# Kernel optimization log

Measured on AMD Instinct MI355X. Metric: run time of the kernel, lower is better.

The kernel has to match this reference:

```python
import jax, jax.numpy as jnp
import numpy as np

UNITS = 512
EPS = 1e-6

def setup_inputs() -> dict:
    key = jax.random.key(0)
    x = jax.random.normal(key, (262144, UNITS), dtype=jnp.float32)
    return {"x": x}

def reference(x):
    d = x.shape[1]
    # Gram matrix with diagonal jitter: [d, d]
    g = x.T @ x + jnp.eye(d, dtype=x.dtype) * EPS
    L = jnp.linalg.cholesky(g)  # lower triangular [d, d]
    # inv(L) via triangular solve (same math as tf.linalg.inv on L)
    L_inv = jax.scipy.linalg.solve_triangular(L, jnp.eye(d, dtype=x.dtype), lower=True)
    ortho_weights = L_inv.T * jnp.sqrt(jnp.float32(UNITS))
    return x @ ortho_weights
```

## Files before the change

kernel.cpp:

```cpp
#include <hip/hip_runtime.h>


#define EPSJ 1e-6f
#define SQRTD 22.627416997969522f

typedef short bf16x8 __attribute__((ext_vector_type(8)));
typedef float f32x4 __attribute__((ext_vector_type(4)));

__device__ __forceinline__ unsigned short f2bf(float f) {
  unsigned u = __float_as_uint(f);
  unsigned r = u + 0x7fffu + ((u >> 16) & 1u);
  return (unsigned short)(r >> 16);
}

__device__ __forceinline__ int swz(int row, int slot) {
  return slot ^ ((row ^ (row >> 3)) & 7);
}

#define GLOAD16(g, l)                                                         \
  __builtin_amdgcn_global_load_lds(                                           \
      (const __attribute__((address_space(1))) void*)(g),                     \
      (__attribute__((address_space(3))) void*)(l), 16, 0, 0)

__global__ __launch_bounds__(512, 2) void gram_k1(
    const float* __restrict__ X, unsigned short* __restrict__ Xbf,
    float* __restrict__ part, int nchunk) {
  __shared__ unsigned short As[256 * 64];
  __shared__ unsigned short Bs[256 * 64];
  const int b = blockIdx.x;
  const int s0 = (int)((long)4096 * b / nchunk);
  const int s1 = (int)((long)4096 * (b + 1) / nchunk);
  const int t = threadIdx.x, lane = t & 63, w = t >> 6;
  const int wr = w >> 2, wc = w & 3;
  const int kg = t >> 6;
  const int c = t & 63;
  unsigned short* half = (c < 32) ? As : Bs;
  const int cl = (c & 31) * 8;

  f32x4 acc[8][4];
  const f32x4 zf = {0.f, 0.f, 0.f, 0.f};
  #pragma unroll
  for (int a = 0; a < 8; ++a)
    #pragma unroll
    for (int bb = 0; bb < 4; ++bb) acc[a][bb] = zf;

  for (int ks = s0; ks < s1; ++ks) {
    long r0 = (long)ks * 64 + kg * 8;
    const float* src = X + r0 * 512 + c * 8;
    uint4 rp[8];
    #pragma unroll
    for (int rr = 0; rr < 8; ++rr) {
      float4 f0 = *(const float4*)(src + rr * 512);
      float4 f1 = *(const float4*)(src + rr * 512 + 4);
      rp[rr].x = (unsigned)f2bf(f0.x) | ((unsigned)f2bf(f0.y) << 16);
      rp[rr].y = (unsigned)f2bf(f0.z) | ((unsigned)f2bf(f0.w) << 16);
      rp[rr].z = (unsigned)f2bf(f1.x) | ((unsigned)f2bf(f1.y) << 16);
      rp[rr].w = (unsigned)f2bf(f1.z) | ((unsigned)f2bf(f1.w) << 16);
      *(uint4*)(Xbf + (r0 + rr) * 512 + c * 8) = rp[rr];
    }
    #pragma unroll
    for (int s = 0; s < 8; ++s) {
      unsigned v[8];
      #pragma unroll
      for (int rr = 0; rr < 8; ++rr) {
        unsigned word = (s & 4) ? ((s & 2) ? rp[rr].w : rp[rr].z)
                                : ((s & 2) ? rp[rr].y : rp[rr].x);
        v[rr] = (s & 1) ? (word >> 16) : (word & 0xFFFFu);
      }
      uint4 o = make_uint4(v[0] | (v[1] << 16), v[2] | (v[3] << 16),
                           v[4] | (v[5] << 16), v[6] | (v[7] << 16));
      int cc = cl + s;
      int sl = kg ^ ((cc ^ (cc >> 3)) & 7);
      *(uint4*)((char*)half + cc * 128 + sl * 16) = o;
    }
    __syncthreads();
    #pragma unroll
    for (int kk = 0; kk < 2; ++kk) {
      bf16x8 af[8], bfr[4];
      #pragma unroll
      for (int fm = 0; fm < 8; ++fm) {
        int row = wr * 128 + fm * 16 + (lane & 15);
        af[fm] = *(const bf16x8*)((const char*)As + row * 128 +
                                  swz(row, kk * 4 + (lane >> 4)) * 16);
      }
      #pragma unroll
      for (int fn = 0; fn < 4; ++fn) {
        int row = wc * 64 + fn * 16 + (lane & 15);
        bfr[fn] = *(const bf16x8*)((const char*)Bs + row * 128 +
                                   swz(row, kk * 4 + (lane >> 4)) * 16);
      }
      #pragma unroll
      for (int fm = 0; fm < 8; ++fm)
        #pragma unroll
        for (int fn = 0; fn < 4; ++fn)
          acc[fm][fn] = __builtin_amdgcn_mfma_f32_16x16x32_bf16(
              bfr[fn], af[fm], acc[fm][fn], 0, 0, 0);
    }
    __syncthreads();
  }
  float* out = part + (long)(b * 3 + 2) * 65536;
  #pragma unroll
  for (int fm = 0; fm < 8; ++fm)
    #pragma unroll
    for (int fn = 0; fn < 4; ++fn) {
      int mi = wr * 128 + fm * 16 + (lane & 15);
      int nj = wc * 64 + fn * 16 + (lane >> 4) * 4;
      *(float4*)(out + mi * 256 + nj) = *(float4*)&acc[fm][fn];
    }
}

__device__ __forceinline__ void stage_pack4(
    const unsigned short* __restrict__ src, unsigned short* dst, int c0,
    int kg) {
  uint4 r0 = *(const uint4*)src;
  uint4 r1 = *(const uint4*)(src + 512);
  uint4 r2 = *(const uint4*)(src + 1024);
  uint4 r3 = *(const uint4*)(src + 1536);
  unsigned a[4] = {r0.x, r0.y, r0.z, r0.w};
  unsigned b[4] = {r1.x, r1.y, r1.z, r1.w};
  unsigned c[4] = {r2.x, r2.y, r2.z, r2.w};
  unsigned d[4] = {r3.x, r3.y, r3.z, r3.w};
  const int khi = kg >> 1, koff = (kg & 1) * 8;
  #pragma unroll
  for (int s = 0; s < 8; ++s) {
    int wsel = s >> 1, sh = (s & 1) * 16;
    unsigned v0 = (a[wsel] >> sh) & 0xFFFFu;
    unsigned v1 = (b[wsel] >> sh) & 0xFFFFu;
    unsigned v2 = (c[wsel] >> sh) & 0xFFFFu;
    unsigned v3 = (d[wsel] >> sh) & 0xFFFFu;
    int cc = c0 + s;
    int sl = khi ^ ((cc ^ (cc >> 3)) & 7);
    *(uint2*)((char*)dst + cc * 128 + sl * 16 + koff) =
        make_uint2(v0 | (v1 << 16), v2 | (v3 << 16));
  }
}

__global__ __launch_bounds__(512, 2) void gram_k2(
    const unsigned short* __restrict__ Xbf, float* __restrict__ part,
    int nchunk) {
  __shared__ unsigned short As[256 * 64];
  const int b = blockIdx.x, pos = b & 1, chunk = b >> 1;
  const int s0 = (int)((long)4096 * chunk / nchunk);
  const int s1 = (int)((long)4096 * (chunk + 1) / nchunk);
  const int ca = pos ? 256 : 0;
  const int t = threadIdx.x, lane = t & 63, w = t >> 6;
  const int wr = w >> 2, wc = w & 3;

  f32x4 acc[8][4];
  const f32x4 zf = {0.f, 0.f, 0.f, 0.f};
  #pragma unroll
  for (int a = 0; a < 8; ++a)
    #pragma unroll
    for (int bb = 0; bb < 4; ++bb) acc[a][bb] = zf;

  const int c0 = (t & 31) * 8;
  const int kg = t >> 5;

  for (int ks = s0; ks < s1; ++ks) {
    long r = (long)ks * 64 + kg * 4;
    stage_pack4(Xbf + r * 512 + ca + c0, As, c0, kg);
    __syncthreads();
    #pragma unroll
    for (int kk = 0; kk < 2; ++kk) {
      bf16x8 af[8], bfr[4];
      #pragma unroll
      for (int fm = 0; fm < 8; ++fm) {
        int row = wr * 128 + fm * 16 + (lane & 15);
        af[fm] = *(const bf16x8*)((const char*)As + row * 128 +
                                  swz(row, kk * 4 + (lane >> 4)) * 16);
      }
      #pragma unroll
      for (int fn = 0; fn < 4; ++fn) {
        int row = wc * 64 + fn * 16 + (lane & 15);
        bfr[fn] = *(const bf16x8*)((const char*)As + row * 128 +
                                   swz(row, kk * 4 + (lane >> 4)) * 16);
      }
      #pragma unroll
      for (int fm = 0; fm < 8; ++fm)
        #pragma unroll
        for (int fn = 0; fn < 4; ++fn)
          acc[fm][fn] = __builtin_amdgcn_mfma_f32_16x16x32_bf16(
              bfr[fn], af[fm], acc[fm][fn], 0, 0, 0);
    }
    __syncthreads();
  }
  float* out = part + (long)(chunk * 3 + pos) * 65536;
  #pragma unroll
  for (int fm = 0; fm < 8; ++fm)
    #pragma unroll
    for (int fn = 0; fn < 4; ++fn) {
      int mi = wr * 128 + fm * 16 + (lane & 15);
      int nj = wc * 64 + fn * 16 + (lane >> 4) * 4;
      *(float4*)(out + mi * 256 + nj) = *(float4*)&acc[fm][fn];
    }
}

__global__ __launch_bounds__(512, 2) void gram_f32(
    const float* __restrict__ X, float* __restrict__ part, int nchunk) {
  __shared__ unsigned short As[256 * 64];
  __shared__ unsigned short Bs[256 * 64];
  const int b = blockIdx.x;
  const int pos = b % 3;
  const int chunk = b / 3;
  const int CR = 262144 / nchunk;
  const long r0 = (long)chunk * CR;
  const int ca = (pos == 1) ? 256 : 0;
  const int cb = (pos == 0) ? 0 : 256;
  const bool diag = (pos != 2);
  const int t = threadIdx.x, lane = t & 63, w = t >> 6;
  const int wr = w >> 2, wc = w & 3;

  f32x4 acc[8][4];
  const f32x4 zf = {0.f, 0.f, 0.f, 0.f};
  #pragma unroll
  for (int a = 0; a < 8; ++a)
    #pragma unroll
    for (int bb = 0; bb < 4; ++bb) acc[a][bb] = zf;

  const int c_oct = t & 31, msub = t >> 5;

  for (int ks = 0; ks < CR; ks += 64) {
    #pragma unroll
    for (int it = 0; it < 4; ++it) {
      int m = msub + 16 * it;
      long row = r0 + ks + m;
      const float4* sa = (const float4*)(X + row * 512 + ca + c_oct * 8);
      float4 a0 = sa[0], a1 = sa[1];
      {
        float v[8] = {a0.x, a0.y, a0.z, a0.w, a1.x, a1.y, a1.z, a1.w};
        #pragma unroll
        for (int s = 0; s < 8; ++s) {
          int cc = c_oct * 8 + s;
          int off = cc * 128 + ((2 * m) ^ (((cc ^ (cc >> 3)) & 7) << 4));
          *(unsigned short*)((char*)As + off) = f2bf(v[s]);
        }
      }
      if (!diag) {
        const float4* sb = (const float4*)(X + row * 512 + cb + c_oct * 8);
        float4 b0 = sb[0], b1 = sb[1];
        float v[8] = {b0.x, b0.y, b0.z, b0.w, b1.x, b1.y, b1.z, b1.w};
        #pragma unroll
        for (int s = 0; s < 8; ++s) {
          int cc = c_oct * 8 + s;
          int off = cc * 128 + ((2 * m) ^ (((cc ^ (cc >> 3)) & 7) << 4));
          *(unsigned short*)((char*)Bs + off) = f2bf(v[s]);
        }
      }
    }
    __syncthreads();
    const unsigned short* Bp = diag ? As : Bs;
    #pragma unroll
    for (int kk = 0; kk < 2; ++kk) {
      bf16x8 af[8], bfr[4];
      #pragma unroll
      for (int fm = 0; fm < 8; ++fm) {
        int row = wr * 128 + fm * 16 + (lane & 15);
        af[fm] = *(const bf16x8*)((const char*)As + row * 128 +
                                  swz(row, kk * 4 + (lane >> 4)) * 16);
      }
      #pragma unroll
      for (int fn = 0; fn < 4; ++fn) {
        int row = wc * 64 + fn * 16 + (lane & 15);
        bfr[fn] = *(const bf16x8*)((const char*)Bp + row * 128 +
                                   swz(row, kk * 4 + (lane >> 4)) * 16);
      }
      #pragma unroll
      for (int fm = 0; fm < 8; ++fm)
        #pragma unroll
        for (int fn = 0; fn < 4; ++fn)
          acc[fm][fn] = __builtin_amdgcn_mfma_f32_16x16x32_bf16(
              bfr[fn], af[fm], acc[fm][fn], 0, 0, 0);
    }
    __syncthreads();
  }
  float* out = part + (long)b * 65536;
  #pragma unroll
  for (int fm = 0; fm < 8; ++fm)
    #pragma unroll
    for (int fn = 0; fn < 4; ++fn) {
      int mi = wr * 128 + fm * 16 + (lane & 15);
      int nj = wc * 64 + fn * 16 + (lane >> 4) * 4;
      *(float4*)(out + mi * 256 + nj) = *(float4*)&acc[fm][fn];
    }
}

__global__ void gram_reduce(const float* __restrict__ part,
                            float* __restrict__ G, int nchunk) {
  int idx = blockIdx.x * 256 + threadIdx.x;
  int pos = idx >> 16;
  int e = idx & 65535;
  float s = 0.f;
  for (int ch = 0; ch < nchunk; ++ch)
    s += part[(long)(ch * 3 + pos) * 65536 + e];
  int i = e >> 8, j = e & 255;
  if (pos == 0) {
    G[i * 512 + j] = s;
  } else if (pos == 1) {
    G[(256 + i) * 512 + 256 + j] = s;
  } else {
    G[i * 512 + 256 + j] = s;
    G[(256 + j) * 512 + i] = s;
  }
}

__global__ __launch_bounds__(256) void chol_step(float* __restrict__ G,
                                                 float* __restrict__ Dinv,
                                                 int p) {
  __shared__ float Pb[64][65];
  __shared__ float Sb[64][65];
  __shared__ float Inv[64][65];
  __shared__ float SbP[64][65];
  __shared__ float Ub[64][65];
  __shared__ float Tt[32][33];
  const int t = threadIdx.x;
  const int r0 = 64 * p;
  const int tr = (t >> 4) * 4, tc = (t & 15) * 4;

  for (int idx = t; idx < 4096; idx += 256) {
    int i = idx >> 6, j = idx & 63;
    float v = G[(long)(r0 + i) * 512 + r0 + j];
    if (i == j) v += EPSJ;
    Pb[i][j] = v;
  }
  __syncthreads();

  if (p > 0) {
    float cc[4][4] = {{0.f}};
    for (int r = 0; r < p; ++r) {
      for (int idx = t; idx < 4096; idx += 256) {
        int i = idx >> 6, j = idx & 63;
        Sb[i][j] = G[(long)(r0 + i) * 512 + 64 * r + j];
      }
      __syncthreads();
      #pragma unroll 4
      for (int k = 0; k < 64; ++k) {
        float a0 = Sb[tr][k], a1 = Sb[tr+1][k], a2 = Sb[tr+2][k], a3 = Sb[tr+3][k];
        float b0 = Sb[tc][k], b1 = Sb[tc+1][k], b2 = Sb[tc+2][k], b3 = Sb[tc+3][k];
        cc[0][0]+=a0*b0; cc[0][1]+=a0*b1; cc[0][2]+=a0*b2; cc[0][3]+=a0*b3;
        cc[1][0]+=a1*b0; cc[1][1]+=a1*b1; cc[1][2]+=a1*b2; cc[1][3]+=a1*b3;
        cc[2][0]+=a2*b0; cc[2][1]+=a2*b1; cc[2][2]+=a2*b2; cc[2][3]+=a2*b3;
        cc[3][0]+=a3*b0; cc[3][1]+=a3*b1; cc[3][2]+=a3*b2; cc[3][3]+=a3*b3;
      }
      __syncthreads();
    }
    #pragma unroll
    for (int u = 0; u < 4; ++u)
      #pragma unroll
      for (int v = 0; v < 4; ++v)
        Pb[tr + u][tc + v] -= cc[u][v];
    __syncthreads();
  }

  const int lane = t & 63, w = t >> 6;
  #pragma unroll
  for (int sp = 0; sp < 2; ++sp) {
    const int b0 = sp * 32;
    if (w == 0) {
      float rr[32];
      #pragma unroll
      for (int k = 0; k < 32; ++k)
        rr[k] = (lane < 32) ? Pb[b0 + lane][b0 + k] : 0.f;
      #pragma unroll
      for (int j = 0; j < 32; ++j) {
        float d = sqrtf(__shfl(rr[j], j));
        if (lane == j) rr[j] = d;
        else if (lane > j && lane < 32) rr[j] = rr[j] / d;
        float rj = rr[j];
        #pragma unroll
        for (int k = j + 1; k < 32; ++k) {
          float Lkj = __shfl(rj, k);
          if (lane > j && lane < 32) rr[k] -= rj * Lkj;
        }
      }
      #pragma unroll
      for (int k = 0; k < 32; ++k)
        if (lane < 32) Pb[b0 + lane][b0 + k] = rr[k];
    }
    __syncthreads();
    if (sp == 0) {
      if (t < 32) {
        int rw = 32 + t;
        float x[32];
        #pragma unroll
        for (int j = 0; j < 32; ++j) x[j] = Pb[rw][j];
        #pragma unroll
        for (int j = 0; j < 32; ++j) {
          float xj = x[j] / Pb[j][j];
          x[j] = xj;
          #pragma unroll
          for (int k2 = j + 1; k2 < 32; ++k2) x[k2] -= xj * Pb[k2][j];
        }
        #pragma unroll
        for (int j = 0; j < 32; ++j) Pb[rw][j] = x[j];
      }
      __syncthreads();
      {
        int i = 32 + (t >> 3), kb = 32 + (t & 7) * 4;
        float sv[4];
        #pragma unroll
        for (int e = 0; e < 4; ++e) sv[e] = Pb[i][kb + e];
        #pragma unroll 4
        for (int j = 0; j < 32; ++j) {
          float aij = Pb[i][j];
          #pragma unroll
          for (int e = 0; e < 4; ++e) sv[e] -= aij * Pb[kb + e][j];
        }
        #pragma unroll
        for (int e = 0; e < 4; ++e) Pb[i][kb + e] = sv[e];
      }
      __syncthreads();
    }
  }

  if (t < 64) {
    int col = t & 31, o = (t >> 5) * 32;
    float x[32];
    #pragma unroll
    for (int i = 0; i < 32; ++i) {
      float s = (i == col) ? 1.f : 0.f;
      #pragma unroll
      for (int j = 0; j < i; ++j) s -= Pb[o + i][o + j] * x[j];
      x[i] = s / Pb[o + i][o + i];
    }
    #pragma unroll
    for (int i = 0; i < 32; ++i) Inv[o + i][o + col] = x[i];
  }
  for (int idx = t; idx < 1024; idx += 256)
    Inv[idx >> 5][32 + (idx & 31)] = 0.f;
  __syncthreads();
  {
    int i = t >> 3, jb = (t & 7) * 4;
    float sv[4] = {0.f, 0.f, 0.f, 0.f};
    #pragma unroll 4
    for (int k = 0; k < 32; ++k) {
      float bik = Pb[32 + i][k];
      #pragma unroll
      for (int e = 0; e < 4; ++e) sv[e] += bik * Inv[k][jb + e];
    }
    #pragma unroll
    for (int e = 0; e < 4; ++e) Tt[i][jb + e] = sv[e];
  }
  __syncthreads();
  {
    int i = t >> 3, jb = (t & 7) * 4;
    float sv[4] = {0.f, 0.f, 0.f, 0.f};
    #pragma unroll 4
    for (int k = 0; k < 32; ++k) {
      float cik = Inv[32 + i][32 + k];
      #pragma unroll
      for (int e = 0; e < 4; ++e) sv[e] += cik * Tt[k][jb + e];
    }
    #pragma unroll
    for (int e = 0; e < 4; ++e) Inv[32 + i][jb + e] = -sv[e];
  }
  __syncthreads();

  if (blockIdx.x == 0) {
    for (int idx = t; idx < 4096; idx += 256)
      Dinv[p * 4096 + idx] = Inv[idx >> 6][idx & 63];
    return;
  }

  const long rI = 64 * (p + blockIdx.x), cP = 64 * p;
  float cc2[4][4] = {{0.f}};
  for (int r = 0; r < p; ++r) {
    __syncthreads();
    for (int idx = t; idx < 4096; idx += 256) {
      int i = idx >> 6, j = idx & 63;
      Sb[i][j] = G[(rI + i) * 512 + 64 * r + j];
      SbP[i][j] = G[(cP + i) * 512 + 64 * r + j];
    }
    __syncthreads();
    #pragma unroll 4
    for (int k = 0; k < 64; ++k) {
      float a0 = Sb[tr][k], a1 = Sb[tr+1][k], a2 = Sb[tr+2][k], a3 = Sb[tr+3][k];
      float b0 = SbP[tc][k], b1 = SbP[tc+1][k], b2 = SbP[tc+2][k], b3 = SbP[tc+3][k];
      cc2[0][0]+=a0*b0; cc2[0][1]+=a0*b1; cc2[0][2]+=a0*b2; cc2[0][3]+=a0*b3;
      cc2[1][0]+=a1*b0; cc2[1][1]+=a1*b1; cc2[1][2]+=a1*b2; cc2[1][3]+=a1*b3;
      cc2[2][0]+=a2*b0; cc2[2][1]+=a2*b1; cc2[2][2]+=a2*b2; cc2[2][3]+=a2*b3;
      cc2[3][0]+=a3*b0; cc2[3][1]+=a3*b1; cc2[3][2]+=a3*b2; cc2[3][3]+=a3*b3;
    }
  }
  __syncthreads();
  #pragma unroll
  for (int u = 0; u < 4; ++u)
    #pragma unroll
    for (int v = 0; v < 4; ++v)
      Ub[tr + u][tc + v] = G[(rI + tr + u) * 512 + cP + tc + v] - cc2[u][v];
  __syncthreads();
  float xx[4][4] = {{0.f}};
  #pragma unroll 4
  for (int k = 0; k < 64; ++k) {
    float a0 = Ub[tr][k], a1 = Ub[tr+1][k], a2 = Ub[tr+2][k], a3 = Ub[tr+3][k];
    float b0 = Inv[tc][k], b1 = Inv[tc+1][k], b2 = Inv[tc+2][k], b3 = Inv[tc+3][k];
    xx[0][0]+=a0*b0; xx[0][1]+=a0*b1; xx[0][2]+=a0*b2; xx[0][3]+=a0*b3;
    xx[1][0]+=a1*b0; xx[1][1]+=a1*b1; xx[1][2]+=a1*b2; xx[1][3]+=a1*b3;
    xx[2][0]+=a2*b0; xx[2][1]+=a2*b1; xx[2][2]+=a2*b2; xx[2][3]+=a2*b3;
    xx[3][0]+=a3*b0; xx[3][1]+=a3*b1; xx[3][2]+=a3*b2; xx[3][3]+=a3*b3;
  }
  #pragma unroll
  for (int u = 0; u < 4; ++u)
    #pragma unroll
    for (int v = 0; v < 4; ++v)
      G[(rI + tr + u) * 512 + cP + tc + v] = xx[u][v];
}

__global__ __launch_bounds__(256) void tri_assemble(
    const float* __restrict__ G, const float* __restrict__ Dinv,
    unsigned short* __restrict__ Wt) {
  __shared__ float Bsh[448 * 64];
  __shared__ float T[64 * 64];
  const int q = blockIdx.x, t = threadIdx.x;
  const int or_ = (t >> 4) * 4, oc = (t & 15) * 4;

  for (int p = q + 1; p < 8; ++p) {
    float cc[4][4] = {{0.f}};
    for (int r = q; r < p; ++r) {
      const float* Lbase = G + (long)(64 * p) * 512 + 64 * r;
      #pragma unroll 4
      for (int k = 0; k < 64; ++k) {
        float a0 = Lbase[(or_ + 0) * 512 + k];
        float a1 = Lbase[(or_ + 1) * 512 + k];
        float a2 = Lbase[(or_ + 2) * 512 + k];
        float a3 = Lbase[(or_ + 3) * 512 + k];
        float b0, b1, b2, b3;
        if (r == q) {
          const float* Bq = Dinv + q * 4096 + k * 64 + oc;
          b0 = Bq[0]; b1 = Bq[1]; b2 = Bq[2]; b3 = Bq[3];
        } else {
          const float* Br = Bsh + ((r - q - 1) * 64 + k) * 64 + oc;
          b0 = Br[0]; b1 = Br[1]; b2 = Br[2]; b3 = Br[3];
        }
        cc[0][0] += a0*b0; cc[0][1] += a0*b1; cc[0][2] += a0*b2; cc[0][3] += a0*b3;
        cc[1][0] += a1*b0; cc[1][1] += a1*b1; cc[1][2] += a1*b2; cc[1][3] += a1*b3;
        cc[2][0] += a2*b0; cc[2][1] += a2*b1; cc[2][2] += a2*b2; cc[2][3] += a2*b3;
        cc[3][0] += a3*b0; cc[3][1] += a3*b1; cc[3][2] += a3*b2; cc[3][3] += a3*b3;
      }
    }
    #pragma unroll
    for (int u = 0; u < 4; ++u)
      #pragma unroll
      for (int v = 0; v < 4; ++v)
        T[(or_ + u) * 64 + oc + v] = cc[u][v];
    __syncthreads();

    float c2[4][4] = {{0.f}};
    const float* Dp = Dinv + p * 4096;
    #pragma unroll 4
    for (int k = 0; k < 64; ++k) {
      float a0 = Dp[(or_ + 0) * 64 + k];
      float a1 = Dp[(or_ + 1) * 64 + k];
      float a2 = Dp[(or_ + 2) * 64 + k];
      float a3 = Dp[(or_ + 3) * 64 + k];
      const float* Tk = T + k * 64 + oc;
      float b0 = Tk[0], b1 = Tk[1], b2 = Tk[2], b3 = Tk[3];
      c2[0][0] += a0*b0; c2[0][1] += a0*b1; c2[0][2] += a0*b2; c2[0][3] += a0*b3;
      c2[1][0] += a1*b0; c2[1][1] += a1*b1; c2[1][2] += a1*b2; c2[1][3] += a1*b3;
      c2[2][0] += a2*b0; c2[2][1] += a2*b1; c2[2][2] += a2*b2; c2[2][3] += a2*b3;
      c2[3][0] += a3*b0; c2[3][1] += a3*b1; c2[3][2] += a3*b2; c2[3][3] += a3*b3;
    }
    #pragma unroll
    for (int u = 0; u < 4; ++u)
      #pragma unroll
      for (int v = 0; v < 4; ++v)
        Bsh[((p - q - 1) * 64 + or_ + u) * 64 + oc + v] = -c2[u][v];
    __syncthreads();
  }

  const int nr = (8 - q) * 64;
  for (int idx = t; idx < nr * 64; idx += 256) {
    int i = idx >> 6, kk = idx & 63;
    float v = (i < 64) ? Dinv[q * 4096 + i * 64 + kk]
                       : Bsh[(i - 64) * 64 + kk];
    int n = 64 * q + i;
    Wt[(long)n * 512 + 64 * q + kk] = f2bf(SQRTD * v);
  }
  for (int idx = t; idx < 64 * q * 64; idx += 256) {
    int n = idx >> 6, kk = idx & 63;
    Wt[(long)n * 512 + 64 * q + kk] = 0;
  }
}

__global__ __launch_bounds__(512, 4) void ymm5(
    const unsigned short* __restrict__ Xbf,
    const unsigned short* __restrict__ Wt, float* __restrict__ Y) {
  __shared__ unsigned short As[2][128 * 64];
  __shared__ unsigned short Bs[2][128 * 64];
  const int t = threadIdx.x, lane = t & 63, w = t >> 6;
  const int id = blockIdx.x;
  const int xcd = id & 7, j = id >> 3;
  const long m0 = (long)((j >> 2) * 8 + xcd) * 128;
  const int n0 = (j & 3) * 128;
  const int wm = (w >> 1) * 32, wn = (w & 1) * 64;
  f32x4 acc[2][4];
  const f32x4 zf = {0.f, 0.f, 0.f, 0.f};
  #pragma unroll
  for (int a = 0; a < 2; ++a)
    #pragma unroll
    for (int bq = 0; bq < 4; ++bq) acc[a][bq] = zf;

  auto stage = [&](int buf, int k0) {
    #pragma unroll
    for (int h = 0; h < 2; ++h) {
      int seg = t + h * 512;
      int row = seg >> 3, sl = seg & 7;
      const unsigned short* sA =
          Xbf + (m0 + row) * 512 + k0 + swz(row, sl) * 8;
      const unsigned short* sB =
          Wt + (long)(n0 + row) * 512 + k0 + swz(row, sl) * 8;
      GLOAD16(sA, &As[buf][seg * 8]);
      GLOAD16(sB, &Bs[buf][seg * 8]);
    }
  };
  auto compute = [&](int buf) {
    #pragma unroll
    for (int kk = 0; kk < 2; ++kk) {
      bf16x8 af[2], bfr[4];
      #pragma unroll
      for (int fm = 0; fm < 2; ++fm) {
        int row = wm + fm * 16 + (lane & 15);
        af[fm] = *(const bf16x8*)((const char*)As[buf] + row * 128 +
                                  swz(row, kk * 4 + (lane >> 4)) * 16);
      }
      #pragma unroll
      for (int fn = 0; fn < 4; ++fn) {
        int row = wn + fn * 16 + (lane & 15);
        bfr[fn] = *(const bf16x8*)((const char*)Bs[buf] + row * 128 +
                                   swz(row, kk * 4 + (lane >> 4)) * 16);
      }
      #pragma unroll
      for (int fm = 0; fm < 2; ++fm)
        #pragma unroll
        for (int fn = 0; fn < 4; ++fn)
          acc[fm][fn] = __builtin_amdgcn_mfma_f32_16x16x32_bf16(
              bfr[fn], af[fm], acc[fm][fn], 0, 0, 0);
    }
  };

  stage(0, 0);
  asm volatile("s_waitcnt vmcnt(0)" ::: "memory");
  __builtin_amdgcn_s_barrier();
  int cur = 0;
  #pragma unroll 1
  for (int kt = 0; kt < 7; ++kt) {
    stage(cur ^ 1, (kt + 1) * 64);
    asm volatile("s_waitcnt vmcnt(4)" ::: "memory");
    __builtin_amdgcn_sched_barrier(0);
    __builtin_amdgcn_s_barrier();
    compute(cur);
    __builtin_amdgcn_s_barrier();
    cur ^= 1;
  }
  asm volatile("s_waitcnt vmcnt(0)" ::: "memory");
  __builtin_amdgcn_sched_barrier(0);
  __builtin_amdgcn_s_barrier();
  compute(cur);

  #pragma unroll
  for (int fm = 0; fm < 2; ++fm)
    #pragma unroll
    for (int fn = 0; fn < 4; ++fn) {
      long row = m0 + wm + fm * 16 + (lane & 15);
      int col = n0 + wn + fn * 16 + (lane >> 4) * 4;
      *(float4*)(Y + row * 512 + col) = *(float4*)&acc[fm][fn];
    }
}

__global__ __launch_bounds__(256) void ymm_v1(const float* __restrict__ X,
                                              const unsigned short* __restrict__ Wt,
                                              float* __restrict__ Y) {
  __shared__ unsigned short As[128 * 64];
  __shared__ unsigned short Bs[128 * 64];
  const int t = threadIdx.x, lane = t & 63, w = t >> 6;
  const long m0 = (long)blockIdx.x * 128;
  const int n0 = blockIdx.y * 128;
  const int wm = (w >> 1) * 64, wn = (w & 1) * 64;
  f32x4 acc[4][4];
  const f32x4 zf = {0.f, 0.f, 0.f, 0.f};
  #pragma unroll
  for (int a = 0; a < 4; ++a)
    #pragma unroll
    for (int bq = 0; bq < 4; ++bq) acc[a][bq] = zf;
  const int ko = t & 7, mrow = t >> 3;

  for (int k0 = 0; k0 < 512; k0 += 64) {
    #pragma unroll
    for (int it = 0; it < 4; ++it) {
      int m = mrow + 32 * it;
      const float4* src = (const float4*)(X + (m0 + m) * 512 + k0 + ko * 8);
      float4 f0 = src[0], f1 = src[1];
      unsigned p0 = (unsigned)f2bf(f0.x) | ((unsigned)f2bf(f0.y) << 16);
      unsigned p1 = (unsigned)f2bf(f0.z) | ((unsigned)f2bf(f0.w) << 16);
      unsigned p2 = (unsigned)f2bf(f1.x) | ((unsigned)f2bf(f1.y) << 16);
      unsigned p3 = (unsigned)f2bf(f1.z) | ((unsigned)f2bf(f1.w) << 16);
      int slot = swz(m, ko);
      *(uint4*)((char*)As + m * 128 + slot * 16) = make_uint4(p0, p1, p2, p3);
    }
    #pragma unroll
    for (int it = 0; it < 4; ++it) {
      int n = mrow + 32 * it;
      uint4 raw = *(const uint4*)(Wt + (long)(n0 + n) * 512 + k0 + ko * 8);
      int slot = swz(n, ko);
      *(uint4*)((char*)Bs + n * 128 + slot * 16) = raw;
    }
    __syncthreads();
    #pragma unroll
    for (int kk = 0; kk < 2; ++kk) {
      bf16x8 af[4], bfr[4];
      #pragma unroll
      for (int fm = 0; fm < 4; ++fm) {
        int row = wm + fm * 16 + (lane & 15);
        af[fm] = *(const bf16x8*)((const char*)As + row * 128 +
                                  swz(row, kk * 4 + (lane >> 4)) * 16);
      }
      #pragma unroll
      for (int fn = 0; fn < 4; ++fn) {
        int row = wn + fn * 16 + (lane & 15);
        bfr[fn] = *(const bf16x8*)((const char*)Bs + row * 128 +
                                   swz(row, kk * 4 + (lane >> 4)) * 16);
      }
      #pragma unroll
      for (int fm = 0; fm < 4; ++fm)
        #pragma unroll
        for (int fn = 0; fn < 4; ++fn)
          acc[fm][fn] = __builtin_amdgcn_mfma_f32_16x16x32_bf16(
              af[fm], bfr[fn], acc[fm][fn], 0, 0, 0);
    }
    __syncthreads();
  }
  #pragma unroll
  for (int fm = 0; fm < 4; ++fm)
    #pragma unroll
    for (int fn = 0; fn < 4; ++fn)
      #pragma unroll
      for (int j = 0; j < 4; ++j) {
        long row = m0 + wm + fm * 16 + (lane >> 4) * 4 + j;
        int col = n0 + wn + fn * 16 + (lane & 15);
        Y[row * 512 + col] = acc[fm][fn][j];
      }
}

extern "C" void kernel_launch(void* const* d_in, const int* in_sizes, int n_in,
                              void* d_out, int out_size, void* d_ws, size_t ws_size,
                              hipStream_t stream) {
  const float* X = (const float*)d_in[0];
  float* Y = (float*)d_out;
  char* ws = (char*)d_ws;
  float* G = (float*)ws;
  unsigned short* Wt = (unsigned short*)(ws + (1 << 20));
  float* Dinv = (float*)(ws + (1 << 20) + (1 << 19));

  const int NCH = 255;
  size_t part_off = (size_t)(2 << 20);
  size_t part_bytes = (size_t)NCH * 3 * 65536 * 4;
  size_t xbf_off = part_off + part_bytes;
  size_t need = xbf_off + (size_t)134217728 * 2;

  if (ws_size >= need) {
    float* part = (float*)(ws + part_off);
    unsigned short* Xbf = (unsigned short*)(ws + xbf_off);
    gram_k1<<<NCH, 512, 0, stream>>>(X, Xbf, part, NCH);
    gram_k2<<<2 * NCH, 512, 0, stream>>>(Xbf, part, NCH);
    gram_reduce<<<768, 256, 0, stream>>>(part, G, NCH);
    for (int p = 0; p < 8; ++p)
      chol_step<<<8 - p, 256, 0, stream>>>(G, Dinv, p);
    tri_assemble<<<8, 256, 0, stream>>>(G, Dinv, Wt);
    ymm5<<<8192, 512, 0, stream>>>(Xbf, Wt, Y);
  } else {
    float* part = (float*)(ws + part_off);
    size_t fixed = part_off;
    int nchunk = 64;
    while (nchunk > 1 && fixed + (size_t)nchunk * 3 * 65536 * 4 > ws_size)
      nchunk >>= 1;
    gram_f32<<<3 * nchunk, 512, 0, stream>>>(X, part, nchunk);
    gram_reduce<<<768, 256, 0, stream>>>(part, G, nchunk);
    for (int p = 0; p < 8; ++p)
      chol_step<<<8 - p, 256, 0, stream>>>(G, Dinv, p);
    tri_assemble<<<8, 256, 0, stream>>>(G, Dinv, Wt);
    ymm_v1<<<dim3(2048, 4), 256, 0, stream>>>(X, Wt, Y);
  }
}
```

Before: 1.581 ms.

## Split blocked Cholesky step into diagonal and panel kernels, tweak ymm barriers

Each Cholesky step is split into two launches. A single-block kernel factors and inverts the 64x64 diagonal block, then writes the factored block and its inverse to global memory. A second kernel then updates the trailing panel blocks using the stored inverse. Before, every block of the step redundantly recomputed the diagonal factorization. In exchange the number of launches roughly doubles. The ymm kernel also drops its sched_barriers and adds an lgkmcnt wait before the second barrier.

```diff
diff --git a/kernel.cpp b/kernel.cpp
--- a/kernel.cpp
+++ b/kernel.cpp
@@ -15,6 +15,12 @@
 
 __device__ __forceinline__ int swz(int row, int slot) {
   return slot ^ ((row ^ (row >> 3)) & 7);
+}
+
+__device__ __forceinline__ float wred(float s) {
+  s += __shfl_xor(s, 1);  s += __shfl_xor(s, 2);  s += __shfl_xor(s, 4);
+  s += __shfl_xor(s, 8);  s += __shfl_xor(s, 16); s += __shfl_xor(s, 32);
+  return s;
 }
 
 #define GLOAD16(g, l)                                                         \
@@ -255,14 +261,14 @@
       #pragma unroll
       for (int fm = 0; fm < 8; ++fm) {
         int row = wr * 128 + fm * 16 + (lane & 15);
-        af[fm] = *(const bf16x8*)((const char*)As + row * 128 +
-                                  swz(row, kk * 4 + (lane >> 4)) * 16);
+        int slot = swz(row, kk * 4 + (lane >> 4));
+        af[fm] = *(const bf16x8*)((const char*)As + row * 128 + slot * 16);
       }
       #pragma unroll
       for (int fn = 0; fn < 4; ++fn) {
         int row = wc * 64 + fn * 16 + (lane & 15);
-        bfr[fn] = *(const bf16x8*)((const char*)Bp + row * 128 +
-                                   swz(row, kk * 4 + (lane >> 4)) * 16);
+        int slot = swz(row, kk * 4 + (lane >> 4));
+        bfr[fn] = *(const bf16x8*)((const char*)Bp + row * 128 + slot * 16);
       }
       #pragma unroll
       for (int fm = 0; fm < 8; ++fm)
@@ -303,14 +309,12 @@
   }
 }
 
-__global__ __launch_bounds__(256) void chol_step(float* __restrict__ G,
-                                                 float* __restrict__ Dinv,
-                                                 int p) {
+__global__ __launch_bounds__(256) void chol_d64(float* __restrict__ G,
+                                                float* __restrict__ Dinv,
+                                                int p) {
   __shared__ float Pb[64][65];
   __shared__ float Sb[64][65];
   __shared__ float Inv[64][65];
-  __shared__ float SbP[64][65];
-  __shared__ float Ub[64][65];
   __shared__ float Tt[32][33];
   const int t = threadIdx.x;
   const int r0 = 64 * p;
@@ -454,31 +458,44 @@
     for (int e = 0; e < 4; ++e) Inv[32 + i][jb + e] = -sv[e];
   }
   __syncthreads();
-
-  if (blockIdx.x == 0) {
-    for (int idx = t; idx < 4096; idx += 256)
-      Dinv[p * 4096 + idx] = Inv[idx >> 6][idx & 63];
-    return;
-  }
-
-  const long rI = 64 * (p + blockIdx.x), cP = 64 * p;
-  float cc2[4][4] = {{0.f}};
+  for (int idx = t; idx < 4096; idx += 256) {
+    int i = idx >> 6, j = idx & 63;
+    G[(long)(r0 + i) * 512 + r0 + j] = Pb[i][j];
+    Dinv[p * 4096 + idx] = Inv[i][j];
+  }
+}
+
+__global__ __launch_bounds__(256) void chol_t64(float* __restrict__ G,
+                                                const float* __restrict__ Dinv,
+                                                int p) {
+  __shared__ float SbI[64][65];
+  __shared__ float SbP[64][65];
+  __shared__ float Ub[64][65];
+  __shared__ float Db[64][65];
+  const int t = threadIdx.x;
+  const long rI = 64 * (p + 1 + blockIdx.x), cP = 64 * p;
+  const int tr = (t >> 4) * 4, tc = (t & 15) * 4;
+
+  for (int idx = t; idx < 4096; idx += 256)
+    Db[idx >> 6][idx & 63] = Dinv[p * 4096 + idx];
+
+  float cc[4][4] = {{0.f}};
   for (int r = 0; r < p; ++r) {
     __syncthreads();
     for (int idx = t; idx < 4096; idx += 256) {
       int i = idx >> 6, j = idx & 63;
-      Sb[i][j] = G[(rI + i) * 512 + 64 * r + j];
+      SbI[i][j] = G[(rI + i) * 512 + 64 * r + j];
       SbP[i][j] = G[(cP + i) * 512 + 64 * r + j];
     }
     __syncthreads();
     #pragma unroll 4
     for (int k = 0; k < 64; ++k) {
-      float a0 = Sb[tr][k], a1 = Sb[tr+1][k], a2 = Sb[tr+2][k], a3 = Sb[tr+3][k];
+      float a0 = SbI[tr][k], a1 = SbI[tr+1][k], a2 = SbI[tr+2][k], a3 = SbI[tr+3][k];
       float b0 = SbP[tc][k], b1 = SbP[tc+1][k], b2 = SbP[tc+2][k], b3 = SbP[tc+3][k];
-      cc2[0][0]+=a0*b0; cc2[0][1]+=a0*b1; cc2[0][2]+=a0*b2; cc2[0][3]+=a0*b3;
-      cc2[1][0]+=a1*b0; cc2[1][1]+=a1*b1; cc2[1][2]+=a1*b2; cc2[1][3]+=a1*b3;
-      cc2[2][0]+=a2*b0; cc2[2][1]+=a2*b1; cc2[2][2]+=a2*b2; cc2[2][3]+=a2*b3;
-      cc2[3][0]+=a3*b0; cc2[3][1]+=a3*b1; cc2[3][2]+=a3*b2; cc2[3][3]+=a3*b3;
+      cc[0][0]+=a0*b0; cc[0][1]+=a0*b1; cc[0][2]+=a0*b2; cc[0][3]+=a0*b3;
+      cc[1][0]+=a1*b0; cc[1][1]+=a1*b1; cc[1][2]+=a1*b2; cc[1][3]+=a1*b3;
+      cc[2][0]+=a2*b0; cc[2][1]+=a2*b1; cc[2][2]+=a2*b2; cc[2][3]+=a2*b3;
+      cc[3][0]+=a3*b0; cc[3][1]+=a3*b1; cc[3][2]+=a3*b2; cc[3][3]+=a3*b3;
     }
   }
   __syncthreads();
@@ -486,13 +503,14 @@
   for (int u = 0; u < 4; ++u)
     #pragma unroll
     for (int v = 0; v < 4; ++v)
-      Ub[tr + u][tc + v] = G[(rI + tr + u) * 512 + cP + tc + v] - cc2[u][v];
+      Ub[tr + u][tc + v] =
+          G[(rI + tr + u) * 512 + cP + tc + v] - cc[u][v];
   __syncthreads();
   float xx[4][4] = {{0.f}};
   #pragma unroll 4
   for (int k = 0; k < 64; ++k) {
     float a0 = Ub[tr][k], a1 = Ub[tr+1][k], a2 = Ub[tr+2][k], a3 = Ub[tr+3][k];
-    float b0 = Inv[tc][k], b1 = Inv[tc+1][k], b2 = Inv[tc+2][k], b3 = Inv[tc+3][k];
+    float b0 = Db[tc][k], b1 = Db[tc+1][k], b2 = Db[tc+2][k], b3 = Db[tc+3][k];
     xx[0][0]+=a0*b0; xx[0][1]+=a0*b1; xx[0][2]+=a0*b2; xx[0][3]+=a0*b3;
     xx[1][0]+=a1*b0; xx[1][1]+=a1*b1; xx[1][2]+=a1*b2; xx[1][3]+=a1*b3;
     xx[2][0]+=a2*b0; xx[2][1]+=a2*b1; xx[2][2]+=a2*b2; xx[2][3]+=a2*b3;
@@ -581,7 +599,7 @@
   }
 }
 
-__global__ __launch_bounds__(512, 4) void ymm5(
+__global__ __launch_bounds__(512, 4) void ymm7(
     const unsigned short* __restrict__ Xbf,
     const unsigned short* __restrict__ Wt, float* __restrict__ Y) {
   __shared__ unsigned short As[2][128 * 64];
@@ -645,14 +663,13 @@
   for (int kt = 0; kt < 7; ++kt) {
     stage(cur ^ 1, (kt + 1) * 64);
     asm volatile("s_waitcnt vmcnt(4)" ::: "memory");
-    __builtin_amdgcn_sched_barrier(0);
     __builtin_amdgcn_s_barrier();
     compute(cur);
+    asm volatile("s_waitcnt lgkmcnt(0)" ::: "memory");
     __builtin_amdgcn_s_barrier();
     cur ^= 1;
   }
   asm volatile("s_waitcnt vmcnt(0)" ::: "memory");
-  __builtin_amdgcn_sched_barrier(0);
   __builtin_amdgcn_s_barrier();
   compute(cur);
 
@@ -740,6 +757,13 @@
       }
 }
 
+static void chol_chain(float* G, float* Dinv, hipStream_t stream) {
+  for (int p = 0; p < 8; ++p) {
+    chol_d64<<<1, 256, 0, stream>>>(G, Dinv, p);
+    if (p < 7) chol_t64<<<7 - p, 256, 0, stream>>>(G, Dinv, p);
+  }
+}
+
 extern "C" void kernel_launch(void* const* d_in, const int* in_sizes, int n_in,
                               void* d_out, int out_size, void* d_ws, size_t ws_size,
                               hipStream_t stream) {
@@ -762,10 +786,9 @@
     gram_k1<<<NCH, 512, 0, stream>>>(X, Xbf, part, NCH);
     gram_k2<<<2 * NCH, 512, 0, stream>>>(Xbf, part, NCH);
     gram_reduce<<<768, 256, 0, stream>>>(part, G, NCH);
-    for (int p = 0; p < 8; ++p)
-      chol_step<<<8 - p, 256, 0, stream>>>(G, Dinv, p);
+    chol_chain(G, Dinv, stream);
     tri_assemble<<<8, 256, 0, stream>>>(G, Dinv, Wt);
-    ymm5<<<8192, 512, 0, stream>>>(Xbf, Wt, Y);
+    ymm7<<<8192, 512, 0, stream>>>(Xbf, Wt, Y);
   } else {
     float* part = (float*)(ws + part_off);
     size_t fixed = part_off;
@@ -774,8 +797,7 @@
       nchunk >>= 1;
     gram_f32<<<3 * nchunk, 512, 0, stream>>>(X, part, nchunk);
     gram_reduce<<<768, 256, 0, stream>>>(part, G, nchunk);
-    for (int p = 0; p < 8; ++p)
-      chol_step<<<8 - p, 256, 0, stream>>>(G, Dinv, p);
+    chol_chain(G, Dinv, stream);
     tri_assemble<<<8, 256, 0, stream>>>(G, Dinv, Wt);
     ymm_v1<<<dim3(2048, 4), 256, 0, stream>>>(X, Wt, Y);
   }
```

After: 1.532 ms. -3.1%, faster.
